# Optimization experiments

Measured on AMD Instinct MI355X. Metric: run time of the kernel, lower is better.

## Reference

```python
import jax, jax.numpy as jnp
import numpy as np

N_NODES = 100000
N_EDGES = 1600000
IN_CH, HID_CH, OUT_CH = 128, 64, 40


def setup_inputs() -> dict:
    key = jax.random.key(0)
    k_x, k_e, k_w1, k_w2 = jax.random.split(key, 4)
    x = jax.random.normal(k_x, (N_NODES, IN_CH), dtype=jnp.float32)
    edge_index = jax.random.randint(k_e, (2, N_EDGES), 0, N_NODES, dtype=jnp.int64)
    # Glorot-ish scaled weights, zero bias (matches GCNConv init convention)
    W1 = jax.random.normal(k_w1, (IN_CH, HID_CH), dtype=jnp.float32) / np.sqrt(IN_CH)
    b1 = jnp.zeros((HID_CH,), dtype=jnp.float32)
    W2 = jax.random.normal(k_w2, (HID_CH, OUT_CH), dtype=jnp.float32) / np.sqrt(HID_CH)
    b2 = jnp.zeros((OUT_CH,), dtype=jnp.float32)
    return {"x": x, "edge_index": edge_index, "W1": W1, "b1": b1, "W2": W2, "b2": b2}


def _gcn_conv(x, edge_index, W, b, n):
    """GCNConv with normalize=True: linear transform, add self-loops,
    symmetric D^-1/2 A D^-1/2 aggregation (source_to_target flow), bias."""
    h = x @ W  # [n, out]
    loops = jnp.arange(n, dtype=edge_index.dtype)
    row = jnp.concatenate([edge_index[0], loops])  # sources
    col = jnp.concatenate([edge_index[1], loops])  # targets
    deg = jax.ops.segment_sum(jnp.ones_like(col, dtype=h.dtype), col, num_segments=n)
    dinv = jnp.where(deg > 0, jax.lax.rsqrt(deg), jnp.zeros_like(deg))
    w = dinv[row] * dinv[col]  # [E+n] per-edge norm
    out = jax.ops.segment_sum(h[row] * w[:, None], col, num_segments=n)  # scatter-add to targets
    return out + b


def reference(x, edge_index, W1, b1, W2, b2):
    # eval mode: F.dropout(p=0.8, training=False) is identity
    n = x.shape[0]
    h = jax.nn.relu(_gcn_conv(x, edge_index, W1, b1, n))
    return _gcn_conv(h, edge_index, W2, b2, n)  # [N, OUT_CH] logits
```

## Files before the change

kernel.cpp:

```cpp
#include <hip/hip_runtime.h>

#define N_NODES 100000
#define NPAD    100032
#define N_EDGES 1600000
#define IN_CH   128
#define HID_CH  64
#define OUT_CH  40
#define NBKT    196
#define EPB     4096
#define CAP     9216
#define CAPC    10752

using bf16x8 = __attribute__((ext_vector_type(8))) short;
using f32x4  = __attribute__((ext_vector_type(4))) float;

__device__ __forceinline__ float bf2f(unsigned short u) {
    union { unsigned int i; float f; } c; c.i = ((unsigned int)u) << 16; return c.f;
}
__device__ __forceinline__ unsigned short f2bf(float f) {
    union { float f; unsigned int i; } c; c.f = f;
    unsigned int r = c.i + 0x7FFFu + ((c.i >> 16) & 1u);
    return (unsigned short)(r >> 16);
}
__device__ __forceinline__ float4 bf2f4(ushort4 u) {
    return make_float4(bf2f(u.x), bf2f(u.y), bf2f(u.z), bf2f(u.w));
}

__global__ void k_bin(const int* __restrict__ ei, int* __restrict__ gcur,
                      int* __restrict__ ebuf) {
    __shared__ int hist[NBKT];
    __shared__ int lcur[NBKT];
    int tid = threadIdx.x;
    int base = blockIdx.x * EPB;
    int nloc = N_EDGES - base;
    if (nloc > EPB) nloc = EPB;
    int n4 = nloc >> 2;
    const int4* S4 = (const int4*)(ei + base);
    const int4* D4 = (const int4*)(ei + N_EDGES + base);

    if (tid < NBKT) { hist[tid] = 0; }
    __syncthreads();
    for (int i = tid; i < n4; i += 256) {
        int4 d = D4[i];
        atomicAdd(&hist[d.x >> 9], 1);
        atomicAdd(&hist[d.y >> 9], 1);
        atomicAdd(&hist[d.z >> 9], 1);
        atomicAdd(&hist[d.w >> 9], 1);
    }
    __syncthreads();
    if (tid < NBKT) {
        int h = hist[tid];
        lcur[tid] = h ? (tid * CAP + atomicAdd(&gcur[tid], h)) : 0;
    }
    __syncthreads();
    for (int i = tid; i < n4; i += 256) {
        int4 s = S4[i];
        int4 d = D4[i];
        int p;
        p = atomicAdd(&lcur[d.x >> 9], 1); ebuf[p] = s.x | ((d.x & 511) << 17);
        p = atomicAdd(&lcur[d.y >> 9], 1); ebuf[p] = s.y | ((d.y & 511) << 17);
        p = atomicAdd(&lcur[d.z >> 9], 1); ebuf[p] = s.z | ((d.z & 511) << 17);
        p = atomicAdd(&lcur[d.w >> 9], 1); ebuf[p] = s.w | ((d.w & 511) << 17);
    }
}

__global__ void k_node(const int* __restrict__ gcur, const int* __restrict__ ebuf,
                       int* __restrict__ row_start, int* __restrict__ row_end,
                       int* __restrict__ csr_src, float* __restrict__ dinv) {
    __shared__ int cnt[512];
    __shared__ int s[512];
    int tid = threadIdx.x;
    int b = blockIdx.x;
    int node0 = b << 9;
    int lo = b * CAP;
    int lo2 = b * CAPC;
    int hi = lo + gcur[b];
    int n = hi - lo, n4 = n >> 2;
    const int4* E4 = (const int4*)(ebuf + lo);

    cnt[tid] = 0;
    __syncthreads();
    for (int i = tid; i < n4; i += 512) {
        int4 w = E4[i];
        atomicAdd(&cnt[(unsigned)w.x >> 17], 1);
        atomicAdd(&cnt[(unsigned)w.y >> 17], 1);
        atomicAdd(&cnt[(unsigned)w.z >> 17], 1);
        atomicAdd(&cnt[(unsigned)w.w >> 17], 1);
    }
    for (int e = lo + (n4 << 2) + tid; e < hi; e += 512)
        atomicAdd(&cnt[(unsigned)ebuf[e] >> 17], 1);
    __syncthreads();
    int c = cnt[tid];
    int cp = (c + 7) & ~7;
    s[tid] = cp;
    __syncthreads();
#pragma unroll
    for (int off = 1; off < 512; off <<= 1) {
        int tv = (tid >= off) ? s[tid - off] : 0;
        __syncthreads();
        s[tid] += tv;
        __syncthreads();
    }
    int nodestart = lo2 + s[tid] - cp;
    int node = node0 + tid;
    if (node < N_NODES) {
        row_start[node] = nodestart;
        row_end[node]   = nodestart + c;
        dinv[node] = rsqrtf(1.0f + (float)c);
    }
    __syncthreads();
    cnt[tid] = nodestart;
    __syncthreads();
    for (int i = tid; i < n4; i += 512) {
        int4 w = E4[i];
        int p;
        p = atomicAdd(&cnt[(unsigned)w.x >> 17], 1); csr_src[p] = w.x & 0x1FFFF;
        p = atomicAdd(&cnt[(unsigned)w.y >> 17], 1); csr_src[p] = w.y & 0x1FFFF;
        p = atomicAdd(&cnt[(unsigned)w.z >> 17], 1); csr_src[p] = w.z & 0x1FFFF;
        p = atomicAdd(&cnt[(unsigned)w.w >> 17], 1); csr_src[p] = w.w & 0x1FFFF;
    }
    for (int e = lo + (n4 << 2) + tid; e < hi; e += 512) {
        int w = ebuf[e];
        int p = atomicAdd(&cnt[(unsigned)w >> 17], 1);
        csr_src[p] = w & 0x1FFFF;
    }
    for (int p = nodestart + c; p < nodestart + cp; ++p)
        csr_src[p] = N_NODES;
}

__global__ __launch_bounds__(256, 4)
void k_gemm1(const float* __restrict__ x, const float* __restrict__ W1,
             const float* __restrict__ dinv, unsigned short* __restrict__ h1s) {
    __shared__ unsigned short Bl[64 * 136];
    __shared__ float dl[64];
    int tid = threadIdx.x;
    long long node0 = (long long)blockIdx.x * 64;

    for (int i = tid; i < 128 * 64; i += 256) {
        int k = i >> 6, nn = i & 63;
        Bl[nn * 136 + k] = f2bf(W1[i]);
    }
    if (tid < 64) {
        long long gr = node0 + tid;
        dl[tid] = dinv[gr < N_NODES ? gr : N_NODES - 1];
    }
    __syncthreads();

    int lane = tid & 63, wave = tid >> 6;
    int quad = lane >> 4, l16 = lane & 15;
    int arow = wave * 16 + l16;
    long long ga = node0 + arow;
    if (ga >= N_NODES) ga = N_NODES - 1;
    const float* xr = x + ga * IN_CH;
    f32x4 ac0 = {0,0,0,0}, ac1 = {0,0,0,0}, ac2 = {0,0,0,0}, ac3 = {0,0,0,0};

#pragma unroll
    for (int ks = 0; ks < 4; ++ks) {
        int ko = ks * 32 + quad * 8;
        float4 xa = *(const float4*)&xr[ko];
        float4 xb = *(const float4*)&xr[ko + 4];
        bf16x8 a;
        a[0] = (short)f2bf(xa.x); a[1] = (short)f2bf(xa.y);
        a[2] = (short)f2bf(xa.z); a[3] = (short)f2bf(xa.w);
        a[4] = (short)f2bf(xb.x); a[5] = (short)f2bf(xb.y);
        a[6] = (short)f2bf(xb.z); a[7] = (short)f2bf(xb.w);
        bf16x8 b0 = *(const bf16x8*)&Bl[( 0 + l16) * 136 + ko];
        bf16x8 b1 = *(const bf16x8*)&Bl[(16 + l16) * 136 + ko];
        bf16x8 b2 = *(const bf16x8*)&Bl[(32 + l16) * 136 + ko];
        bf16x8 b3 = *(const bf16x8*)&Bl[(48 + l16) * 136 + ko];
        ac0 = __builtin_amdgcn_mfma_f32_16x16x32_bf16(a, b0, ac0, 0, 0, 0);
        ac1 = __builtin_amdgcn_mfma_f32_16x16x32_bf16(a, b1, ac1, 0, 0, 0);
        ac2 = __builtin_amdgcn_mfma_f32_16x16x32_bf16(a, b2, ac2, 0, 0, 0);
        ac3 = __builtin_amdgcn_mfma_f32_16x16x32_bf16(a, b3, ac3, 0, 0, 0);
    }

#pragma unroll
    for (int r = 0; r < 4; ++r) {
        int rl = wave * 16 + quad * 4 + r;
        long long grow = node0 + rl;
        if (grow < N_NODES) {
            float dd = dl[rl];
            h1s[grow * 64 +  0 + l16] = f2bf(ac0[r] * dd);
            h1s[grow * 64 + 16 + l16] = f2bf(ac1[r] * dd);
            h1s[grow * 64 + 32 + l16] = f2bf(ac2[r] * dd);
            h1s[grow * 64 + 48 + l16] = f2bf(ac3[r] * dd);
        } else {
            h1s[grow * 64 +  0 + l16] = 0;
            h1s[grow * 64 + 16 + l16] = 0;
            h1s[grow * 64 + 32 + l16] = 0;
            h1s[grow * 64 + 48 + l16] = 0;
        }
    }
}

__global__ __launch_bounds__(256, 4)
void k_agg1g2(const int* __restrict__ row_start, const int* __restrict__ row_end,
              const int* __restrict__ csr_src,
              const unsigned short* __restrict__ h1s, const float* __restrict__ dinv,
              const float* __restrict__ b1, const float* __restrict__ W2,
              unsigned short* __restrict__ h2s) {
    __shared__ unsigned short Al[32 * 72];
    __shared__ unsigned short Bl[48 * 72];
    __shared__ float dl[32];
    int tid = threadIdx.x;
    long long node0 = (long long)blockIdx.x * 32;

    for (int i = tid; i < 48 * 64; i += 256) {
        int nn = i >> 6, k = i & 63;
        Bl[nn * 72 + k] = f2bf(nn < OUT_CH ? W2[k * OUT_CH + nn] : 0.0f);
    }
    if (tid < 32) {
        long long gr = node0 + tid;
        dl[tid] = dinv[gr < N_NODES ? gr : N_NODES - 1];
    }
    __syncthreads();

    int g  = tid >> 4;
    int hh = (tid >> 3) & 1;
    int c8 = tid & 7;
    int nl = g * 2 + hh;
    long long node = node0 + nl;

    int e0 = 0, d = 0;
    if (node < N_NODES) { e0 = row_start[node]; d = row_end[node] - e0; }
    int len8 = (d + 7) & ~7;
    int lenO = __shfl_xor(len8, 8, 16);
    int nIt  = (len8 > lenO ? len8 : lenO) >> 3;

    float4 aA = {0.f,0.f,0.f,0.f}, aB = aA, aC = aA, aD = aA;

    int it = 0;
    while (it < nIt) {
        bool real = (it << 3) < len8;
        int base = real ? (e0 + (it << 3)) : e0;
        int idxr = csr_src[base + c8];
        int s0 = __shfl(idxr, 0, 8), s1 = __shfl(idxr, 1, 8);
        int s2 = __shfl(idxr, 2, 8), s3 = __shfl(idxr, 3, 8);
        int s4 = __shfl(idxr, 4, 8), s5 = __shfl(idxr, 5, 8);
        int s6 = __shfl(idxr, 6, 8), s7 = __shfl(idxr, 7, 8);
        if (!real) { s0=s1=s2=s3=s4=s5=s6=s7 = N_NODES; }
        const unsigned short* Hc = h1s + (long long)c8 * 8;
        bf16x8 r0 = *(const bf16x8*)&Hc[(long long)s0 * 64];
        bf16x8 r1 = *(const bf16x8*)&Hc[(long long)s1 * 64];
        bf16x8 r2 = *(const bf16x8*)&Hc[(long long)s2 * 64];
        bf16x8 r3 = *(const bf16x8*)&Hc[(long long)s3 * 64];
        bf16x8 r4 = *(const bf16x8*)&Hc[(long long)s4 * 64];
        bf16x8 r5 = *(const bf16x8*)&Hc[(long long)s5 * 64];
        bf16x8 r6 = *(const bf16x8*)&Hc[(long long)s6 * 64];
        bf16x8 r7 = *(const bf16x8*)&Hc[(long long)s7 * 64];
#define ACC8(R, LO, HI) { \
        LO.x += bf2f((unsigned short)R[0]); LO.y += bf2f((unsigned short)R[1]); \
        LO.z += bf2f((unsigned short)R[2]); LO.w += bf2f((unsigned short)R[3]); \
        HI.x += bf2f((unsigned short)R[4]); HI.y += bf2f((unsigned short)R[5]); \
        HI.z += bf2f((unsigned short)R[6]); HI.w += bf2f((unsigned short)R[7]); }
        ACC8(r0, aA, aB) ACC8(r1, aC, aD)
        ACC8(r2, aA, aB) ACC8(r3, aC, aD)
        ACC8(r4, aA, aB) ACC8(r5, aC, aD)
        ACC8(r6, aA, aB) ACC8(r7, aC, aD)
#undef ACC8
        ++it;
    }
    aA.x += aC.x; aA.y += aC.y; aA.z += aC.z; aA.w += aC.w;
    aB.x += aD.x; aB.y += aD.y; aB.z += aD.z; aB.w += aD.w;

    bf16x8 res = {0,0,0,0,0,0,0,0};
    if (node < N_NODES) {
        bf16x8 sv = *(const bf16x8*)&h1s[(long long)node * 64 + c8 * 8];
        aA.x += bf2f((unsigned short)sv[0]); aA.y += bf2f((unsigned short)sv[1]);
        aA.z += bf2f((unsigned short)sv[2]); aA.w += bf2f((unsigned short)sv[3]);
        aB.x += bf2f((unsigned short)sv[4]); aB.y += bf2f((unsigned short)sv[5]);
        aB.z += bf2f((unsigned short)sv[6]); aB.w += bf2f((unsigned short)sv[7]);
        float dd = dl[nl];
        float4 blo = ((const float4*)b1)[c8 * 2];
        float4 bhi = ((const float4*)b1)[c8 * 2 + 1];
        res[0] = (short)f2bf(fmaxf(aA.x * dd + blo.x, 0.f));
        res[1] = (short)f2bf(fmaxf(aA.y * dd + blo.y, 0.f));
        res[2] = (short)f2bf(fmaxf(aA.z * dd + blo.z, 0.f));
        res[3] = (short)f2bf(fmaxf(aA.w * dd + blo.w, 0.f));
        res[4] = (short)f2bf(fmaxf(aB.x * dd + bhi.x, 0.f));
        res[5] = (short)f2bf(fmaxf(aB.y * dd + bhi.y, 0.f));
        res[6] = (short)f2bf(fmaxf(aB.z * dd + bhi.z, 0.f));
        res[7] = (short)f2bf(fmaxf(aB.w * dd + bhi.w, 0.f));
    }
    *(bf16x8*)&Al[nl * 72 + c8 * 8] = res;
    __syncthreads();

    int lane = tid & 63, wave = tid >> 6;
    if (wave < 2) {
        int quad = lane >> 4, l16 = lane & 15;
        int arow = wave * 16 + l16;
        f32x4 ac0 = {0,0,0,0}, ac1 = {0,0,0,0}, ac2 = {0,0,0,0};

#pragma unroll
        for (int ks = 0; ks < 2; ++ks) {
            int ko = ks * 32 + quad * 8;
            bf16x8 a  = *(const bf16x8*)&Al[arow * 72 + ko];
            bf16x8 b0 = *(const bf16x8*)&Bl[( 0 + l16) * 72 + ko];
            bf16x8 b1v = *(const bf16x8*)&Bl[(16 + l16) * 72 + ko];
            bf16x8 b2 = *(const bf16x8*)&Bl[(32 + l16) * 72 + ko];
            ac0 = __builtin_amdgcn_mfma_f32_16x16x32_bf16(a, b0, ac0, 0, 0, 0);
            ac1 = __builtin_amdgcn_mfma_f32_16x16x32_bf16(a, b1v, ac1, 0, 0, 0);
            ac2 = __builtin_amdgcn_mfma_f32_16x16x32_bf16(a, b2, ac2, 0, 0, 0);
        }

#pragma unroll
        for (int r = 0; r < 4; ++r) {
            int rl = wave * 16 + quad * 4 + r;
            long long grow = node0 + rl;
            if (grow < N_NODES) {
                float dd = dl[rl];
                h2s[grow * 40 +  0 + l16] = f2bf(ac0[r] * dd);
                h2s[grow * 40 + 16 + l16] = f2bf(ac1[r] * dd);
                if (l16 < 8) h2s[grow * 40 + 32 + l16] = f2bf(ac2[r] * dd);
            } else if (grow < NPAD) {
                h2s[grow * 40 +  0 + l16] = 0;
                h2s[grow * 40 + 16 + l16] = 0;
                if (l16 < 8) h2s[grow * 40 + 32 + l16] = 0;
            }
        }
    }
}

__global__ __launch_bounds__(256, 4)
void k_agg2(const int* __restrict__ row_start, const int* __restrict__ row_end,
            const int* __restrict__ csr_src,
            const unsigned short* __restrict__ h2s, const float* __restrict__ dinv,
            const float* __restrict__ b2, float* __restrict__ out) {
    int tid = threadIdx.x;
    long long node0 = (long long)blockIdx.x * 32;

    int g  = tid >> 4;
    int hh = (tid >> 3) & 1;
    int c8 = tid & 7;
    int nl = g * 2 + hh;
    long long node = node0 + nl;
    bool act = c8 < 5;

    int e0 = 0, d = 0;
    if (node < N_NODES) { e0 = row_start[node]; d = row_end[node] - e0; }
    int len8 = (d + 7) & ~7;
    int lenO = __shfl_xor(len8, 8, 16);
    int nIt  = (len8 > lenO ? len8 : lenO) >> 3;

    const unsigned short* Hb = h2s + (act ? (long long)c8 * 8
                                          : (long long)N_NODES * 40);
    long long rmul = act ? 40LL : 0LL;

    float4 aA = {0.f,0.f,0.f,0.f}, aB = aA, aC = aA, aD = aA;

    int it = 0;
    while (it < nIt) {
        bool real = (it << 3) < len8;
        int base = real ? (e0 + (it << 3)) : e0;
        int idxr = csr_src[base + c8];
        int s0 = __shfl(idxr, 0, 8), s1 = __shfl(idxr, 1, 8);
        int s2 = __shfl(idxr, 2, 8), s3 = __shfl(idxr, 3, 8);
        int s4 = __shfl(idxr, 4, 8), s5 = __shfl(idxr, 5, 8);
        int s6 = __shfl(idxr, 6, 8), s7 = __shfl(idxr, 7, 8);
        if (!real) { s0=s1=s2=s3=s4=s5=s6=s7 = N_NODES; }
        bf16x8 r0 = *(const bf16x8*)&Hb[(long long)s0 * rmul];
        bf16x8 r1 = *(const bf16x8*)&Hb[(long long)s1 * rmul];
        bf16x8 r2 = *(const bf16x8*)&Hb[(long long)s2 * rmul];
        bf16x8 r3 = *(const bf16x8*)&Hb[(long long)s3 * rmul];
        bf16x8 r4 = *(const bf16x8*)&Hb[(long long)s4 * rmul];
        bf16x8 r5 = *(const bf16x8*)&Hb[(long long)s5 * rmul];
        bf16x8 r6 = *(const bf16x8*)&Hb[(long long)s6 * rmul];
        bf16x8 r7 = *(const bf16x8*)&Hb[(long long)s7 * rmul];
#define ACC8(R, LO, HI) { \
        LO.x += bf2f((unsigned short)R[0]); LO.y += bf2f((unsigned short)R[1]); \
        LO.z += bf2f((unsigned short)R[2]); LO.w += bf2f((unsigned short)R[3]); \
        HI.x += bf2f((unsigned short)R[4]); HI.y += bf2f((unsigned short)R[5]); \
        HI.z += bf2f((unsigned short)R[6]); HI.w += bf2f((unsigned short)R[7]); }
        ACC8(r0, aA, aB) ACC8(r1, aC, aD)
        ACC8(r2, aA, aB) ACC8(r3, aC, aD)
        ACC8(r4, aA, aB) ACC8(r5, aC, aD)
        ACC8(r6, aA, aB) ACC8(r7, aC, aD)
#undef ACC8
        ++it;
    }
    aA.x += aC.x; aA.y += aC.y; aA.z += aC.z; aA.w += aC.w;
    aB.x += aD.x; aB.y += aD.y; aB.z += aD.z; aB.w += aD.w;

    if (node < N_NODES && act) {
        bf16x8 sv = *(const bf16x8*)&h2s[(long long)node * 40 + c8 * 8];
        aA.x += bf2f((unsigned short)sv[0]); aA.y += bf2f((unsigned short)sv[1]);
        aA.z += bf2f((unsigned short)sv[2]); aA.w += bf2f((unsigned short)sv[3]);
        aB.x += bf2f((unsigned short)sv[4]); aB.y += bf2f((unsigned short)sv[5]);
        aB.z += bf2f((unsigned short)sv[6]); aB.w += bf2f((unsigned short)sv[7]);
        float dd = dinv[node];
        float4 blo = ((const float4*)b2)[c8 * 2];
        float4 bhi = ((const float4*)b2)[c8 * 2 + 1];
        float4 o0, o1;
        o0.x = aA.x * dd + blo.x; o0.y = aA.y * dd + blo.y;
        o0.z = aA.z * dd + blo.z; o0.w = aA.w * dd + blo.w;
        o1.x = aB.x * dd + bhi.x; o1.y = aB.y * dd + bhi.y;
        o1.z = aB.z * dd + bhi.z; o1.w = aB.w * dd + bhi.w;
        float* op = out + node * 40 + c8 * 8;
        *(float4*)op = o0;
        *(float4*)(op + 4) = o1;
    }
}

extern "C" void kernel_launch(void* const* d_in, const int* in_sizes, int n_in,
                              void* d_out, int out_size, void* d_ws, size_t ws_size,
                              hipStream_t stream) {
    const float* x  = (const float*)d_in[0];
    const int*   ei = (const int*)d_in[1];
    const float* W1 = (const float*)d_in[2];
    const float* b1 = (const float*)d_in[3];
    const float* W2 = (const float*)d_in[4];
    const float* b2 = (const float*)d_in[5];
    float* out = (float*)d_out;

    unsigned short* hbuf  = (unsigned short*)d_ws;
    unsigned short* h2buf = hbuf + 64LL * NPAD;
    int* ebuf      = (int*)(h2buf + 40LL * NPAD);
    int* csr_src   = ebuf + NBKT * CAP;
    int* row_start = csr_src + NBKT * CAPC + 64;
    int* row_end   = row_start + N_NODES;
    int* gcur      = row_end + N_NODES;
    float* dinv    = (float*)(gcur + 256);

    const int B = 256;
    const int gRows = NPAD / 64;
    const int gAgg  = NPAD / 32;

    hipMemsetAsync((void*)gcur, 0, NBKT * sizeof(int), stream);
    k_bin<<<(N_EDGES + EPB - 1) / EPB, B, 0, stream>>>(ei, gcur, ebuf);
    k_node<<<NBKT, 512, 0, stream>>>(gcur, ebuf, row_start, row_end, csr_src, dinv);

    k_gemm1<<<gRows, B, 0, stream>>>(x, W1, dinv, hbuf);
    k_agg1g2<<<gAgg, B, 0, stream>>>(row_start, row_end, csr_src, hbuf, dinv,
                                     b1, W2, h2buf);
    k_agg2<<<gAgg, B, 0, stream>>>(row_start, row_end, csr_src, h2buf, dinv, b2, out);
}
```

Baseline: 215.1 us.

## Split h1 into channel-group planes and unfuse layer-1 aggregation from GEMM2

```diff
diff --git a/kernel.cpp b/kernel.cpp
--- a/kernel.cpp
+++ b/kernel.cpp
@@ -174,149 +174,158 @@
         ac3 = __builtin_amdgcn_mfma_f32_16x16x32_bf16(a, b3, ac3, 0, 0, 0);
     }
 
+#define H1SG(ROW, C) h1s[((long long)((C) >> 3)) * (8LL * NPAD) + (ROW) * 8 + ((C) & 7)]
 #pragma unroll
     for (int r = 0; r < 4; ++r) {
         int rl = wave * 16 + quad * 4 + r;
         long long grow = node0 + rl;
         if (grow < N_NODES) {
             float dd = dl[rl];
-            h1s[grow * 64 +  0 + l16] = f2bf(ac0[r] * dd);
-            h1s[grow * 64 + 16 + l16] = f2bf(ac1[r] * dd);
-            h1s[grow * 64 + 32 + l16] = f2bf(ac2[r] * dd);
-            h1s[grow * 64 + 48 + l16] = f2bf(ac3[r] * dd);
+            H1SG(grow,  0 + l16) = f2bf(ac0[r] * dd);
+            H1SG(grow, 16 + l16) = f2bf(ac1[r] * dd);
+            H1SG(grow, 32 + l16) = f2bf(ac2[r] * dd);
+            H1SG(grow, 48 + l16) = f2bf(ac3[r] * dd);
         } else {
-            h1s[grow * 64 +  0 + l16] = 0;
-            h1s[grow * 64 + 16 + l16] = 0;
-            h1s[grow * 64 + 32 + l16] = 0;
-            h1s[grow * 64 + 48 + l16] = 0;
+            H1SG(grow,  0 + l16) = 0;
+            H1SG(grow, 16 + l16) = 0;
+            H1SG(grow, 32 + l16) = 0;
+            H1SG(grow, 48 + l16) = 0;
         }
     }
+#undef H1SG
 }
 
 __global__ __launch_bounds__(256, 4)
-void k_agg1g2(const int* __restrict__ row_start, const int* __restrict__ row_end,
-              const int* __restrict__ csr_src,
-              const unsigned short* __restrict__ h1s, const float* __restrict__ dinv,
-              const float* __restrict__ b1, const float* __restrict__ W2,
-              unsigned short* __restrict__ h2s) {
-    __shared__ unsigned short Al[32 * 72];
+void k_agg1(const int* __restrict__ row_start, const int* __restrict__ row_end,
+            const int* __restrict__ csr_src,
+            const unsigned short* __restrict__ h1s, const float* __restrict__ dinv,
+            const float* __restrict__ b1, unsigned short* __restrict__ a1) {
+    int tid = threadIdx.x;
+    int bid = blockIdx.x;
+    int g    = bid & 7;
+    int tile = bid >> 3;
+    long long node0 = (long long)tile * 32;
+    int half = tid >> 3;
+    int c8   = tid & 7;
+    long long node = node0 + half;
+
+    int e0 = 0, d = 0;
+    if (node < N_NODES) { e0 = row_start[node]; d = row_end[node] - e0; }
+    int nIt = ((d + 7) & ~7) >> 3;
+
+    const unsigned short* Hg = h1s + (long long)g * (8LL * NPAD);
+    float4 aLo = {0.f,0.f,0.f,0.f}, aHi = aLo, bLo = aLo, bHi = aLo;
+
+#define ACCV(R, LO, HI) { \
+    LO.x += bf2f((unsigned short)R[0]); LO.y += bf2f((unsigned short)R[1]); \
+    LO.z += bf2f((unsigned short)R[2]); LO.w += bf2f((unsigned short)R[3]); \
+    HI.x += bf2f((unsigned short)R[4]); HI.y += bf2f((unsigned short)R[5]); \
+    HI.z += bf2f((unsigned short)R[6]); HI.w += bf2f((unsigned short)R[7]); }
+
+    int eb = e0 + c8;
+    int it = 0;
+    while (it + 2 <= nIt) {
+        int sA = csr_src[eb];
+        int sB = csr_src[eb + 8];
+        bf16x8 rA = *(const bf16x8*)&Hg[(long long)sA * 8];
+        bf16x8 rB = *(const bf16x8*)&Hg[(long long)sB * 8];
+        ACCV(rA, aLo, aHi)
+        ACCV(rB, bLo, bHi)
+        eb += 16; it += 2;
+    }
+    if (it < nIt) {
+        int sA = csr_src[eb];
+        bf16x8 rA = *(const bf16x8*)&Hg[(long long)sA * 8];
+        ACCV(rA, aLo, aHi)
+    }
+#undef ACCV
+    aLo.x += bLo.x; aLo.y += bLo.y; aLo.z += bLo.z; aLo.w += bLo.w;
+    aHi.x += bHi.x; aHi.y += bHi.y; aHi.z += bHi.z; aHi.w += bHi.w;
+
+#pragma unroll
+    for (int m = 1; m < 8; m <<= 1) {
+        aLo.x += __shfl_xor(aLo.x, m, 8);
+        aLo.y += __shfl_xor(aLo.y, m, 8);
+        aLo.z += __shfl_xor(aLo.z, m, 8);
+        aLo.w += __shfl_xor(aLo.w, m, 8);
+        aHi.x += __shfl_xor(aHi.x, m, 8);
+        aHi.y += __shfl_xor(aHi.y, m, 8);
+        aHi.z += __shfl_xor(aHi.z, m, 8);
+        aHi.w += __shfl_xor(aHi.w, m, 8);
+    }
+
+    if (c8 == 0 && node < N_NODES) {
+        bf16x8 sv = *(const bf16x8*)&Hg[node * 8];
+        aLo.x += bf2f((unsigned short)sv[0]); aLo.y += bf2f((unsigned short)sv[1]);
+        aLo.z += bf2f((unsigned short)sv[2]); aLo.w += bf2f((unsigned short)sv[3]);
+        aHi.x += bf2f((unsigned short)sv[4]); aHi.y += bf2f((unsigned short)sv[5]);
+        aHi.z += bf2f((unsigned short)sv[6]); aHi.w += bf2f((unsigned short)sv[7]);
+        float dd = dinv[node];
+        float4 blo = ((const float4*)b1)[g * 2];
+        float4 bhi = ((const float4*)b1)[g * 2 + 1];
+        bf16x8 res;
+        res[0] = (short)f2bf(fmaxf(aLo.x * dd + blo.x, 0.f));
+        res[1] = (short)f2bf(fmaxf(aLo.y * dd + blo.y, 0.f));
+        res[2] = (short)f2bf(fmaxf(aLo.z * dd + blo.z, 0.f));
+        res[3] = (short)f2bf(fmaxf(aLo.w * dd + blo.w, 0.f));
+        res[4] = (short)f2bf(fmaxf(aHi.x * dd + bhi.x, 0.f));
+        res[5] = (short)f2bf(fmaxf(aHi.y * dd + bhi.y, 0.f));
+        res[6] = (short)f2bf(fmaxf(aHi.z * dd + bhi.z, 0.f));
+        res[7] = (short)f2bf(fmaxf(aHi.w * dd + bhi.w, 0.f));
+        *(bf16x8*)&a1[node * 64 + g * 8] = res;
+    }
+}
+
+__global__ __launch_bounds__(256, 4)
+void k_gemm2(const unsigned short* __restrict__ a1, const float* __restrict__ W2,
+             const float* __restrict__ dinv, unsigned short* __restrict__ h2s) {
     __shared__ unsigned short Bl[48 * 72];
-    __shared__ float dl[32];
-    int tid = threadIdx.x;
-    long long node0 = (long long)blockIdx.x * 32;
+    __shared__ float dl[64];
+    int tid = threadIdx.x;
+    long long node0 = (long long)blockIdx.x * 64;
 
     for (int i = tid; i < 48 * 64; i += 256) {
         int nn = i >> 6, k = i & 63;
         Bl[nn * 72 + k] = f2bf(nn < OUT_CH ? W2[k * OUT_CH + nn] : 0.0f);
     }
-    if (tid < 32) {
+    if (tid < 64) {
         long long gr = node0 + tid;
         dl[tid] = dinv[gr < N_NODES ? gr : N_NODES - 1];
     }
     __syncthreads();
 
-    int g  = tid >> 4;
-    int hh = (tid >> 3) & 1;
-    int c8 = tid & 7;
-    int nl = g * 2 + hh;
-    long long node = node0 + nl;
-
-    int e0 = 0, d = 0;
-    if (node < N_NODES) { e0 = row_start[node]; d = row_end[node] - e0; }
-    int len8 = (d + 7) & ~7;
-    int lenO = __shfl_xor(len8, 8, 16);
-    int nIt  = (len8 > lenO ? len8 : lenO) >> 3;
-
-    float4 aA = {0.f,0.f,0.f,0.f}, aB = aA, aC = aA, aD = aA;
-
-    int it = 0;
-    while (it < nIt) {
-        bool real = (it << 3) < len8;
-        int base = real ? (e0 + (it << 3)) : e0;
-        int idxr = csr_src[base + c8];
-        int s0 = __shfl(idxr, 0, 8), s1 = __shfl(idxr, 1, 8);
-        int s2 = __shfl(idxr, 2, 8), s3 = __shfl(idxr, 3, 8);
-        int s4 = __shfl(idxr, 4, 8), s5 = __shfl(idxr, 5, 8);
-        int s6 = __shfl(idxr, 6, 8), s7 = __shfl(idxr, 7, 8);
-        if (!real) { s0=s1=s2=s3=s4=s5=s6=s7 = N_NODES; }
-        const unsigned short* Hc = h1s + (long long)c8 * 8;
-        bf16x8 r0 = *(const bf16x8*)&Hc[(long long)s0 * 64];
-        bf16x8 r1 = *(const bf16x8*)&Hc[(long long)s1 * 64];
-        bf16x8 r2 = *(const bf16x8*)&Hc[(long long)s2 * 64];
-        bf16x8 r3 = *(const bf16x8*)&Hc[(long long)s3 * 64];
-        bf16x8 r4 = *(const bf16x8*)&Hc[(long long)s4 * 64];
-        bf16x8 r5 = *(const bf16x8*)&Hc[(long long)s5 * 64];
-        bf16x8 r6 = *(const bf16x8*)&Hc[(long long)s6 * 64];
-        bf16x8 r7 = *(const bf16x8*)&Hc[(long long)s7 * 64];
-#define ACC8(R, LO, HI) { \
-        LO.x += bf2f((unsigned short)R[0]); LO.y += bf2f((unsigned short)R[1]); \
-        LO.z += bf2f((unsigned short)R[2]); LO.w += bf2f((unsigned short)R[3]); \
-        HI.x += bf2f((unsigned short)R[4]); HI.y += bf2f((unsigned short)R[5]); \
-        HI.z += bf2f((unsigned short)R[6]); HI.w += bf2f((unsigned short)R[7]); }
-        ACC8(r0, aA, aB) ACC8(r1, aC, aD)
-        ACC8(r2, aA, aB) ACC8(r3, aC, aD)
-        ACC8(r4, aA, aB) ACC8(r5, aC, aD)
-        ACC8(r6, aA, aB) ACC8(r7, aC, aD)
-#undef ACC8
-        ++it;
-    }
-    aA.x += aC.x; aA.y += aC.y; aA.z += aC.z; aA.w += aC.w;
-    aB.x += aD.x; aB.y += aD.y; aB.z += aD.z; aB.w += aD.w;
-
-    bf16x8 res = {0,0,0,0,0,0,0,0};
-    if (node < N_NODES) {
-        bf16x8 sv = *(const bf16x8*)&h1s[(long long)node * 64 + c8 * 8];
-        aA.x += bf2f((unsigned short)sv[0]); aA.y += bf2f((unsigned short)sv[1]);
-        aA.z += bf2f((unsigned short)sv[2]); aA.w += bf2f((unsigned short)sv[3]);
-        aB.x += bf2f((unsigned short)sv[4]); aB.y += bf2f((unsigned short)sv[5]);
-        aB.z += bf2f((unsigned short)sv[6]); aB.w += bf2f((unsigned short)sv[7]);
-        float dd = dl[nl];
-        float4 blo = ((const float4*)b1)[c8 * 2];
-        float4 bhi = ((const float4*)b1)[c8 * 2 + 1];
-        res[0] = (short)f2bf(fmaxf(aA.x * dd + blo.x, 0.f));
-        res[1] = (short)f2bf(fmaxf(aA.y * dd + blo.y, 0.f));
-        res[2] = (short)f2bf(fmaxf(aA.z * dd + blo.z, 0.f));
-        res[3] = (short)f2bf(fmaxf(aA.w * dd + blo.w, 0.f));
-        res[4] = (short)f2bf(fmaxf(aB.x * dd + bhi.x, 0.f));
-        res[5] = (short)f2bf(fmaxf(aB.y * dd + bhi.y, 0.f));
-        res[6] = (short)f2bf(fmaxf(aB.z * dd + bhi.z, 0.f));
-        res[7] = (short)f2bf(fmaxf(aB.w * dd + bhi.w, 0.f));
-    }
-    *(bf16x8*)&Al[nl * 72 + c8 * 8] = res;
-    __syncthreads();
-
     int lane = tid & 63, wave = tid >> 6;
-    if (wave < 2) {
-        int quad = lane >> 4, l16 = lane & 15;
-        int arow = wave * 16 + l16;
-        f32x4 ac0 = {0,0,0,0}, ac1 = {0,0,0,0}, ac2 = {0,0,0,0};
-
-#pragma unroll
-        for (int ks = 0; ks < 2; ++ks) {
-            int ko = ks * 32 + quad * 8;
-            bf16x8 a  = *(const bf16x8*)&Al[arow * 72 + ko];
-            bf16x8 b0 = *(const bf16x8*)&Bl[( 0 + l16) * 72 + ko];
-            bf16x8 b1v = *(const bf16x8*)&Bl[(16 + l16) * 72 + ko];
-            bf16x8 b2 = *(const bf16x8*)&Bl[(32 + l16) * 72 + ko];
-            ac0 = __builtin_amdgcn_mfma_f32_16x16x32_bf16(a, b0, ac0, 0, 0, 0);
-            ac1 = __builtin_amdgcn_mfma_f32_16x16x32_bf16(a, b1v, ac1, 0, 0, 0);
-            ac2 = __builtin_amdgcn_mfma_f32_16x16x32_bf16(a, b2, ac2, 0, 0, 0);
-        }
-
-#pragma unroll
-        for (int r = 0; r < 4; ++r) {
-            int rl = wave * 16 + quad * 4 + r;
-            long long grow = node0 + rl;
-            if (grow < N_NODES) {
-                float dd = dl[rl];
-                h2s[grow * 40 +  0 + l16] = f2bf(ac0[r] * dd);
-                h2s[grow * 40 + 16 + l16] = f2bf(ac1[r] * dd);
-                if (l16 < 8) h2s[grow * 40 + 32 + l16] = f2bf(ac2[r] * dd);
-            } else if (grow < NPAD) {
-                h2s[grow * 40 +  0 + l16] = 0;
-                h2s[grow * 40 + 16 + l16] = 0;
-                if (l16 < 8) h2s[grow * 40 + 32 + l16] = 0;
-            }
+    int quad = lane >> 4, l16 = lane & 15;
+    int arow = wave * 16 + l16;
+    long long ga = node0 + arow;
+    if (ga >= N_NODES) ga = N_NODES - 1;
+    f32x4 ac0 = {0,0,0,0}, ac1 = {0,0,0,0}, ac2 = {0,0,0,0};
+
+#pragma unroll
+    for (int ks = 0; ks < 2; ++ks) {
+        int ko = ks * 32 + quad * 8;
+        bf16x8 a  = *(const bf16x8*)&a1[ga * 64 + ko];
+        bf16x8 b0 = *(const bf16x8*)&Bl[( 0 + l16) * 72 + ko];
+        bf16x8 b1v = *(const bf16x8*)&Bl[(16 + l16) * 72 + ko];
+        bf16x8 b2 = *(const bf16x8*)&Bl[(32 + l16) * 72 + ko];
+        ac0 = __builtin_amdgcn_mfma_f32_16x16x32_bf16(a, b0, ac0, 0, 0, 0);
+        ac1 = __builtin_amdgcn_mfma_f32_16x16x32_bf16(a, b1v, ac1, 0, 0, 0);
+        ac2 = __builtin_amdgcn_mfma_f32_16x16x32_bf16(a, b2, ac2, 0, 0, 0);
+    }
+
+#pragma unroll
+    for (int r = 0; r < 4; ++r) {
+        int rl = wave * 16 + quad * 4 + r;
+        long long grow = node0 + rl;
+        if (grow < N_NODES) {
+            float dd = dl[rl];
+            h2s[grow * 40 +  0 + l16] = f2bf(ac0[r] * dd);
+            h2s[grow * 40 + 16 + l16] = f2bf(ac1[r] * dd);
+            if (l16 < 8) h2s[grow * 40 + 32 + l16] = f2bf(ac2[r] * dd);
+        } else if (grow < NPAD) {
+            h2s[grow * 40 +  0 + l16] = 0;
+            h2s[grow * 40 + 16 + l16] = 0;
+            if (l16 < 8) h2s[grow * 40 + 32 + l16] = 0;
         }
     }
 }
@@ -413,7 +422,8 @@
     float* out = (float*)d_out;
 
     unsigned short* hbuf  = (unsigned short*)d_ws;
-    unsigned short* h2buf = hbuf + 64LL * NPAD;
+    unsigned short* a1buf = hbuf + 64LL * NPAD;
+    unsigned short* h2buf = a1buf + 64LL * NPAD;
     int* ebuf      = (int*)(h2buf + 40LL * NPAD);
     int* csr_src   = ebuf + NBKT * CAP;
     int* row_start = csr_src + NBKT * CAPC + 64;
@@ -423,14 +433,16 @@
 
     const int B = 256;
     const int gRows = NPAD / 64;
-    const int gAgg  = NPAD / 32;
+    const int gAgg1 = (NPAD / 32) * 8;
+    const int gAgg2 = NPAD / 32;
 
     hipMemsetAsync((void*)gcur, 0, NBKT * sizeof(int), stream);
     k_bin<<<(N_EDGES + EPB - 1) / EPB, B, 0, stream>>>(ei, gcur, ebuf);
     k_node<<<NBKT, 512, 0, stream>>>(gcur, ebuf, row_start, row_end, csr_src, dinv);
 
     k_gemm1<<<gRows, B, 0, stream>>>(x, W1, dinv, hbuf);
-    k_agg1g2<<<gAgg, B, 0, stream>>>(row_start, row_end, csr_src, hbuf, dinv,
-                                     b1, W2, h2buf);
-    k_agg2<<<gAgg, B, 0, stream>>>(row_start, row_end, csr_src, h2buf, dinv, b2, out);
-}
+    k_agg1<<<gAgg1, B, 0, stream>>>(row_start, row_end, csr_src, hbuf, dinv,
+                                    b1, a1buf);
+    k_gemm2<<<gRows, B, 0, stream>>>(a1buf, W2, dinv, h2buf);
+    k_agg2<<<gAgg2, B, 0, stream>>>(row_start, row_end, csr_src, h2buf, dinv, b2, out);
+}
```

New measurement: 250.8 us. 1.17x slower.
